# Kernel tuning notes

Hardware: AMD Instinct MI355X
Metric: run time of the kernel (lower is better)

The kernel has to match this reference:

```python
import jax, jax.numpy as jnp
import numpy as np

N, K, D = 500000, 16, 16


def setup_inputs() -> dict:
    key = jax.random.key(0)
    k1, k2, k3, k4 = jax.random.split(key, 4)
    x = jax.random.normal(k1, (N, D), dtype=jnp.float32)
    # mixture weights: positive, sum to 1, shape (1, K)
    pi = jax.nn.softmax(jax.random.normal(k2, (1, K), dtype=jnp.float32), axis=-1)
    mu = jax.random.normal(k3, (K, 1, D), dtype=jnp.float32)
    # SPD covariance per cluster: A A^T / D + I
    A = jax.random.normal(k4, (K, D, D), dtype=jnp.float32)
    Sigma = jnp.einsum('kde,kfe->kdf', A, A) / D + jnp.eye(D, dtype=jnp.float32)
    return {"x": x, "pi": pi, "mu": mu, "Sigma": Sigma}


def reference(x, pi, mu, Sigma):
    # Batched MultivariateNormal log_prob over K clusters (replaces the
    # Python loop over torch.distributions.MultivariateNormal).
    d = x.shape[-1]
    L = jnp.linalg.cholesky(Sigma)                      # (K, D, D)
    diff = x[None, :, :] - mu                           # (K, N, D) via mu (K,1,D)
    # solve L y = diff^T per cluster -> Mahalanobis = ||y||^2
    y = jax.vmap(lambda Lk, dk: jax.scipy.linalg.solve_triangular(Lk, dk.T, lower=True))(L, diff)  # (K, D, N)
    maha = jnp.sum(y * y, axis=1)                       # (K, N)
    half_logdet = jnp.sum(jnp.log(jnp.diagonal(L, axis1=-2, axis2=-1)), axis=-1)  # (K,)
    log2pi = jnp.log(jnp.asarray(2.0 * np.pi, dtype=x.dtype))
    logp = -0.5 * (maha + d * log2pi) - half_logdet[:, None]  # (K, N)
    res_k = jnp.exp(logp).T * pi                        # (N, K), pi broadcasts from (1,K)
    res = res_k / jnp.sum(res_k, axis=1, keepdims=True)  # (N, K)
    return res
```

## Files before the change

kernel.cpp:

```cpp
#include <hip/hip_runtime.h>
#include <math.h>

#define D 16
#define K 16
#define BLK 256
#define PK_WORDS 96

typedef _Float16 h2 __attribute__((ext_vector_type(2)));

__host__ __device__ constexpr int tri(int i, int j) { return i * (i + 1) / 2 + j; }
__host__ __device__ constexpr int rowoff(int i) {
    int s = 0;
    for (int r = 0; r < i; ++r) s += (r + 2) / 2;
    return s;
}

static __device__ __forceinline__ float fdot2f(h2 a, h2 b, float c) {
#if __has_builtin(__builtin_amdgcn_fdot2)
    return __builtin_amdgcn_fdot2(a, b, c, false);
#else
    return fmaf((float)a.x, (float)b.x, fmaf((float)a.y, (float)b.y, c));
#endif
}

static __device__ __forceinline__ unsigned pack2(float f0, float f1) {
    _Float16 h0 = (_Float16)f0, h1 = (_Float16)f1;
    unsigned short b0 = __builtin_bit_cast(unsigned short, h0);
    unsigned short b1 = __builtin_bit_cast(unsigned short, h1);
    return ((unsigned)b1 << 16) | (unsigned)b0;
}

__global__ __launch_bounds__(64) void gmm_prep(
    const float* __restrict__ pi, const float* __restrict__ mu,
    const float* __restrict__ Sigma, float* __restrict__ P)
{
    const int k = threadIdx.x;
    if (k >= K) return;

    float M[tri(D - 1, D - 1) + 1];

#pragma unroll
    for (int i = 0; i < D; ++i)
#pragma unroll
        for (int j = 0; j <= i; ++j)
            M[tri(i, j)] = Sigma[k * D * D + i * D + j];

    float hl = 0.f;
#pragma unroll
    for (int j = 0; j < D; ++j) {
        float s = M[tri(j, j)];
#pragma unroll
        for (int p = 0; p < j; ++p) s -= M[tri(j, p)] * M[tri(j, p)];
        float ljj = sqrtf(s);
        M[tri(j, j)] = ljj;
        hl += logf(ljj);
        float inv = 1.f / ljj;
#pragma unroll
        for (int i = j + 1; i < D; ++i) {
            float t = M[tri(i, j)];
#pragma unroll
            for (int p = 0; p < j; ++p) t -= M[tri(i, p)] * M[tri(j, p)];
            M[tri(i, j)] = t * inv;
        }
    }

#pragma unroll
    for (int j = 0; j < D; ++j) {
        float ujj = 1.f / M[tri(j, j)];
        M[tri(j, j)] = ujj;
#pragma unroll
        for (int i = j + 1; i < D; ++i) {
            float s = 0.f;
#pragma unroll
            for (int p = j; p < i; ++p) s += M[tri(i, p)] * M[tri(p, j)];
            M[tri(i, j)] = -s / M[tri(i, i)];
        }
    }

    const float invs2 = 0.70710678118654752440f;
    float* Pk = P + k * PK_WORDS;
    unsigned* Pu = (unsigned*)Pk;

    Pk[0] = logf(pi[k]) - hl;
#pragma unroll
    for (int i = 0; i < D; ++i) {
        float acc = 0.f;
#pragma unroll
        for (int j = 0; j <= i; ++j) acc += M[tri(i, j)] * mu[k * D + j];
        Pk[1 + i] = -(acc * invs2);
    }
#pragma unroll
    for (int i = 0; i < D; ++i) {
        const int np = (i + 2) / 2;
#pragma unroll
        for (int p = 0; p < np; ++p) {
            float f0 = M[tri(i, 2 * p)] * invs2;
            float f1 = (2 * p + 1 <= i) ? M[tri(i, 2 * p + 1)] * invs2 : 0.f;
            Pu[17 + rowoff(i) + p] = pack2(f0, f1);
        }
    }
#pragma unroll
    for (int q = 89; q < PK_WORDS; ++q) Pu[q] = 0;
}

__global__ __launch_bounds__(BLK) void gmm_main(
    const float* __restrict__ x, const float* __restrict__ P,
    float* __restrict__ out, int N)
{
    const int tid = threadIdx.x;
    const long long n = (long long)blockIdx.x * BLK + tid;
    const bool ok = n < (long long)N;

    float4 xr0 = {0, 0, 0, 0}, xr1 = xr0, xr2 = xr0, xr3 = xr0;
    if (ok) {
        const float4* p = (const float4*)(x + n * D);
        xr0 = p[0]; xr1 = p[1]; xr2 = p[2]; xr3 = p[3];
    }

    h2 xp[8];
    xp[0] = (h2){(_Float16)xr0.x, (_Float16)xr0.y};
    xp[1] = (h2){(_Float16)xr0.z, (_Float16)xr0.w};
    xp[2] = (h2){(_Float16)xr1.x, (_Float16)xr1.y};
    xp[3] = (h2){(_Float16)xr1.z, (_Float16)xr1.w};
    xp[4] = (h2){(_Float16)xr2.x, (_Float16)xr2.y};
    xp[5] = (h2){(_Float16)xr2.z, (_Float16)xr2.w};
    xp[6] = (h2){(_Float16)xr3.x, (_Float16)xr3.y};
    xp[7] = (h2){(_Float16)xr3.z, (_Float16)xr3.w};

    float r[K];
#pragma unroll
    for (int k = 0; k < K; ++k) {
        const float* __restrict__ Pk = P + k * PK_WORDS;
        const unsigned* __restrict__ Uk = (const unsigned*)(Pk + 17);
        float acc = 0.f;
#pragma unroll
        for (int i = 0; i < D; ++i) {
            float y = Pk[1 + i];
            const int np = (i + 2) / 2;
#pragma unroll
            for (int p = 0; p < np; ++p) {
                h2 u = __builtin_bit_cast(h2, Uk[rowoff(i) + p]);
                y = fdot2f(u, xp[p], y);
            }
            acc = fmaf(y, y, acc);
        }
        r[k] = Pk[0] - acc;
    }

    float mx = r[0];
#pragma unroll
    for (int k = 1; k < K; ++k) mx = fmaxf(mx, r[k]);
    float sum = 0.f;
#pragma unroll
    for (int k = 0; k < K; ++k) {
        float e = __expf(r[k] - mx);
        r[k] = e;
        sum += e;
    }
    float inv = 1.f / sum;
    if (ok) {
        float4* po = (float4*)(out + n * D);
        po[0] = (float4){r[0] * inv,  r[1] * inv,  r[2] * inv,  r[3] * inv};
        po[1] = (float4){r[4] * inv,  r[5] * inv,  r[6] * inv,  r[7] * inv};
        po[2] = (float4){r[8] * inv,  r[9] * inv,  r[10] * inv, r[11] * inv};
        po[3] = (float4){r[12] * inv, r[13] * inv, r[14] * inv, r[15] * inv};
    }
}

extern "C" void kernel_launch(void* const* d_in, const int* in_sizes, int n_in,
                              void* d_out, int out_size, void* d_ws, size_t ws_size,
                              hipStream_t stream) {
    const float* x     = (const float*)d_in[0];
    const float* pi    = (const float*)d_in[1];
    const float* mu    = (const float*)d_in[2];
    const float* Sigma = (const float*)d_in[3];
    float* out = (float*)d_out;
    const int N = in_sizes[0] / D;

    float* P = (float*)d_ws;

    gmm_prep<<<1, 64, 0, stream>>>(pi, mu, Sigma, P);

    const int grid = (N + BLK - 1) / BLK;
    gmm_main<<<grid, BLK, 0, stream>>>(x, P, out, N);
}
```

Before: 118.2 us.

## Compute Mahalanobis triangular products with MFMA 32x32x16 f16 instructions

Replaces the per-thread packed fdot2 triangular matrix-vector products with matrix-core MFMA tiles. The prep kernel lays out the scaled inverse Cholesky factors as MFMA A fragments plus bias tiles. The main kernel stages x rows in LDS as B fragments, runs 16 MFMAs per wave, and reduces the squared outputs with lane shuffles. This moves the dominant ALU work onto matrix cores, at the cost of extra LDS traffic, a block barrier and some wasted zero-padded multiplies.

```diff
diff --git a/kernel.cpp b/kernel.cpp
--- a/kernel.cpp
+++ b/kernel.cpp
@@ -4,24 +4,16 @@
 #define D 16
 #define K 16
 #define BLK 256
-#define PK_WORDS 96
-
+
+#define OFF_A 0
+#define OFF_T 2048
+#define OFF_C 2304
+
+typedef _Float16 f16x8 __attribute__((ext_vector_type(8)));
+typedef float    f32x16 __attribute__((ext_vector_type(16)));
 typedef _Float16 h2 __attribute__((ext_vector_type(2)));
 
 __host__ __device__ constexpr int tri(int i, int j) { return i * (i + 1) / 2 + j; }
-__host__ __device__ constexpr int rowoff(int i) {
-    int s = 0;
-    for (int r = 0; r < i; ++r) s += (r + 2) / 2;
-    return s;
-}
-
-static __device__ __forceinline__ float fdot2f(h2 a, h2 b, float c) {
-#if __has_builtin(__builtin_amdgcn_fdot2)
-    return __builtin_amdgcn_fdot2(a, b, c, false);
-#else
-    return fmaf((float)a.x, (float)b.x, fmaf((float)a.y, (float)b.y, c));
-#endif
-}
 
 static __device__ __forceinline__ unsigned pack2(float f0, float f1) {
     _Float16 h0 = (_Float16)f0, h1 = (_Float16)f1;
@@ -45,16 +37,18 @@
         for (int j = 0; j <= i; ++j)
             M[tri(i, j)] = Sigma[k * D * D + i * D + j];
 
-    float hl = 0.f;
+    float invd[D];
+    float prod = 1.f;
 #pragma unroll
     for (int j = 0; j < D; ++j) {
         float s = M[tri(j, j)];
 #pragma unroll
         for (int p = 0; p < j; ++p) s -= M[tri(j, p)] * M[tri(j, p)];
         float ljj = sqrtf(s);
+        prod *= ljj;
+        float inv = 1.f / ljj;
+        invd[j] = inv;
         M[tri(j, j)] = ljj;
-        hl += logf(ljj);
-        float inv = 1.f / ljj;
 #pragma unroll
         for (int i = j + 1; i < D; ++i) {
             float t = M[tri(i, j)];
@@ -66,57 +60,84 @@
 
 #pragma unroll
     for (int j = 0; j < D; ++j) {
-        float ujj = 1.f / M[tri(j, j)];
-        M[tri(j, j)] = ujj;
+        M[tri(j, j)] = invd[j];
 #pragma unroll
         for (int i = j + 1; i < D; ++i) {
             float s = 0.f;
 #pragma unroll
             for (int p = j; p < i; ++p) s += M[tri(i, p)] * M[tri(p, j)];
-            M[tri(i, j)] = -s / M[tri(i, i)];
+            M[tri(i, j)] = -s * invd[i];
         }
     }
 
     const float invs2 = 0.70710678118654752440f;
-    float* Pk = P + k * PK_WORDS;
-    unsigned* Pu = (unsigned*)Pk;
-
-    Pk[0] = logf(pi[k]) - hl;
+
+    float t[D];
 #pragma unroll
     for (int i = 0; i < D; ++i) {
         float acc = 0.f;
 #pragma unroll
         for (int j = 0; j <= i; ++j) acc += M[tri(i, j)] * mu[k * D + j];
-        Pk[1 + i] = -(acc * invs2);
-    }
-#pragma unroll
-    for (int i = 0; i < D; ++i) {
-        const int np = (i + 2) / 2;
-#pragma unroll
-        for (int p = 0; p < np; ++p) {
-            float f0 = M[tri(i, 2 * p)] * invs2;
-            float f1 = (2 * p + 1 <= i) ? M[tri(i, 2 * p + 1)] * invs2 : 0.f;
-            Pu[17 + rowoff(i) + p] = pack2(f0, f1);
-        }
-    }
-#pragma unroll
-    for (int q = 89; q < PK_WORDS; ++q) Pu[q] = 0;
+        t[i] = acc * invs2;
+    }
+
+    P[OFF_C + k] = logf(pi[k] / prod);
+
+    const int tt = k >> 1;
+    const int hi = (k & 1) * 8;
+#pragma unroll
+    for (int w = 0; w < 2; ++w)
+#pragma unroll
+        for (int ii = 0; ii < 8; ++ii) {
+            int comp = (ii & 3) + 8 * (ii >> 2) + 4 * w;
+            P[OFF_T + tt * 32 + w * 16 + hi + ii] = -t[comp];
+        }
+
+    uint4* PA = (uint4*)(P + OFF_A);
+#pragma unroll
+    for (int mm = 0; mm < 32; ++mm) {
+        int m  = (k & 1) * 16 + (mm & 15) + 32 * (mm >> 4);
+        int rr = m & 15;
+        int kc = (m >> 5) * 8;
+        unsigned dw[4];
+#pragma unroll
+        for (int e = 0; e < 4; ++e) {
+            int c0 = kc + 2 * e, c1 = c0 + 1;
+            float f0 = (c0 <= rr) ? M[tri(rr, c0)] * invs2 : 0.f;
+            float f1 = (c1 <= rr) ? M[tri(rr, c1)] * invs2 : 0.f;
+            dw[e] = pack2(f0, f1);
+        }
+        PA[tt * 64 + m] = make_uint4(dw[0], dw[1], dw[2], dw[3]);
+    }
 }
 
 __global__ __launch_bounds__(BLK) void gmm_main(
     const float* __restrict__ x, const float* __restrict__ P,
     float* __restrict__ out, int N)
 {
-    const int tid = threadIdx.x;
+    const int tid  = threadIdx.x;
+    const int lane = tid & 63;
+    const int wave = tid >> 6;
+    const int cc   = lane & 31;
+    const int w    = lane >> 5;
     const long long n = (long long)blockIdx.x * BLK + tid;
     const bool ok = n < (long long)N;
+
+    __shared__ __align__(16) unsigned short xs[4][64][24];
+    __shared__ __align__(64) float ts[256];
+
+    f16x8 Afr[8];
+#pragma unroll
+    for (int t = 0; t < 8; ++t)
+        Afr[t] = ((const f16x8*)(P + OFF_A))[t * 64 + lane];
+
+    if (tid < 64) ((float4*)ts)[tid] = ((const float4*)(P + OFF_T))[tid];
 
     float4 xr0 = {0, 0, 0, 0}, xr1 = xr0, xr2 = xr0, xr3 = xr0;
     if (ok) {
         const float4* p = (const float4*)(x + n * D);
         xr0 = p[0]; xr1 = p[1]; xr2 = p[2]; xr3 = p[3];
     }
-
     h2 xp[8];
     xp[0] = (h2){(_Float16)xr0.x, (_Float16)xr0.y};
     xp[1] = (h2){(_Float16)xr0.z, (_Float16)xr0.w};
@@ -127,34 +148,59 @@
     xp[6] = (h2){(_Float16)xr3.x, (_Float16)xr3.y};
     xp[7] = (h2){(_Float16)xr3.z, (_Float16)xr3.w};
 
+    uint4* rowq = (uint4*)&xs[wave][lane][0];
+    rowq[0] = make_uint4(__builtin_bit_cast(unsigned, xp[0]),
+                         __builtin_bit_cast(unsigned, xp[1]),
+                         __builtin_bit_cast(unsigned, xp[2]),
+                         __builtin_bit_cast(unsigned, xp[3]));
+    rowq[1] = make_uint4(__builtin_bit_cast(unsigned, xp[4]),
+                         __builtin_bit_cast(unsigned, xp[5]),
+                         __builtin_bit_cast(unsigned, xp[6]),
+                         __builtin_bit_cast(unsigned, xp[7]));
+
+    __syncthreads();
+
+    f16x8 Bfr[2];
+#pragma unroll
+    for (int ct = 0; ct < 2; ++ct)
+        Bfr[ct] = *(const f16x8*)(&xs[wave][ct * 32 + cc][w * 8]);
+
     float r[K];
 #pragma unroll
-    for (int k = 0; k < K; ++k) {
-        const float* __restrict__ Pk = P + k * PK_WORDS;
-        const unsigned* __restrict__ Uk = (const unsigned*)(Pk + 17);
-        float acc = 0.f;
-#pragma unroll
-        for (int i = 0; i < D; ++i) {
-            float y = Pk[1 + i];
-            const int np = (i + 2) / 2;
-#pragma unroll
-            for (int p = 0; p < np; ++p) {
-                h2 u = __builtin_bit_cast(h2, Uk[rowoff(i) + p]);
-                y = fdot2f(u, xp[p], y);
-            }
-            acc = fmaf(y, y, acc);
-        }
-        r[k] = Pk[0] - acc;
-    }
+    for (int t = 0; t < 8; ++t) {
+        f32x16 ci = *(const f32x16*)(&ts[t * 32 + w * 16]);
+#pragma unroll
+        for (int ct = 0; ct < 2; ++ct) {
+            f32x16 a = __builtin_amdgcn_mfma_f32_32x32x16_f16(
+                Afr[t], Bfr[ct], ci, 0, 0, 0);
+            float q0 = fmaf(a[0], a[0], a[1] * a[1]);
+            float q1 = fmaf(a[2], a[2], a[3] * a[3]);
+            float q2 = fmaf(a[4], a[4], a[5] * a[5]);
+            float q3 = fmaf(a[6], a[6], a[7] * a[7]);
+            float pA = (q0 + q1) + (q2 + q3);
+            float q4 = fmaf(a[8],  a[8],  a[9]  * a[9]);
+            float q5 = fmaf(a[10], a[10], a[11] * a[11]);
+            float q6 = fmaf(a[12], a[12], a[13] * a[13]);
+            float q7 = fmaf(a[14], a[14], a[15] * a[15]);
+            float pB = (q4 + q5) + (q6 + q7);
+            pA += __shfl_xor(pA, 32);
+            pB += __shfl_xor(pB, 32);
+            if (ct == w) { r[2 * t] = pA; r[2 * t + 1] = pB; }
+        }
+    }
+
+    const float* __restrict__ Pc = P + OFF_C;
+#pragma unroll
+    for (int kk = 0; kk < K; ++kk) r[kk] = Pc[kk] - r[kk];
 
     float mx = r[0];
 #pragma unroll
-    for (int k = 1; k < K; ++k) mx = fmaxf(mx, r[k]);
+    for (int kk = 1; kk < K; ++kk) mx = fmaxf(mx, r[kk]);
     float sum = 0.f;
 #pragma unroll
-    for (int k = 0; k < K; ++k) {
-        float e = __expf(r[k] - mx);
-        r[k] = e;
+    for (int kk = 0; kk < K; ++kk) {
+        float e = __expf(r[kk] - mx);
+        r[kk] = e;
         sum += e;
     }
     float inv = 1.f / sum;
```

Result: faster. 104.2 us (median of 2 runs) (-11.9%).
